# Performance work log

Measured on AMD Instinct MI355X. Metric: run time of the kernel, lower is better.

Reference implementation:

```python
import jax, jax.numpy as jnp
import numpy as np


def setup_inputs() -> dict:
    key = jax.random.key(0)
    k1, k2, k3, k4 = jax.random.split(key, 4)
    bs, h, qlen, slen, dk = 2, 16, 1024, 1024, 64
    q = jax.random.normal(k1, (bs, h, qlen, dk), dtype=jnp.float32)
    k = jax.random.normal(k2, (bs, h, dk, slen), dtype=jnp.float32)
    v = jax.random.normal(k3, (bs, h, slen, dk), dtype=jnp.float32)
    prev = jax.random.normal(k4, (bs, h, qlen, slen), dtype=jnp.float32)
    # scale param = head_dim ** -0.5 (lsa=False -> fixed, not trained)
    scale = jnp.asarray(dk ** (-0.5), dtype=jnp.float32)
    return {"q": q, "k": k, "v": v, "prev": prev, "scale": scale}


def reference(q, k, v, prev, scale):
    # attn_scores = (q @ k) * scale + prev   [bs, h, q_len, seq_len]
    attn_scores = jnp.einsum("bhqd,bhds->bhqs", q, k) * scale + prev
    # no attn_mask / key_padding_mask; dropout p=0.0 -> identity
    attn_weights = jax.nn.softmax(attn_scores, axis=-1)
    # output = attn_weights @ v   [bs, h, q_len, d_v]
    output = jnp.einsum("bhqs,bhsd->bhqd", attn_weights, v)
    # res_attention=True -> also return scores
    return output, attn_weights, attn_scores
```

## Files before the change

### kernel.cpp

```cpp
#include <hip/hip_runtime.h>
#include <hip/hip_bf16.h>

#define BH 32
#define L  1024
#define D  64
#define QT 16

typedef __bf16 bf16x8 __attribute__((ext_vector_type(8)));
typedef float  f32x4  __attribute__((ext_vector_type(4)));

__global__ __launch_bounds__(256) void prep_kernel(
    const float* __restrict__ q, const float* __restrict__ k,
    const float* __restrict__ v,
    __bf16* __restrict__ qb, __bf16* __restrict__ ktb, __bf16* __restrict__ vtb)
{
  __shared__ __align__(16) __bf16 T[128 * 66];
  const int tid = threadIdx.x;
  const int b = blockIdx.x;

  if (b < 1024) {
    const size_t g = (size_t)b * 256 + tid;
    const float4* qin = (const float4*)q;
    float4 f0 = qin[g * 2];
    float4 f1 = qin[g * 2 + 1];
    union { bf16x8 v8; uint4 u4; } o;
    o.v8[0] = (__bf16)f0.x; o.v8[1] = (__bf16)f0.y;
    o.v8[2] = (__bf16)f0.z; o.v8[3] = (__bf16)f0.w;
    o.v8[4] = (__bf16)f1.x; o.v8[5] = (__bf16)f1.y;
    o.v8[6] = (__bf16)f1.z; o.v8[7] = (__bf16)f1.w;
    *(uint4*)(qb + g * 8) = o.u4;
  } else if (b < 1280) {
    const int bb = b - 1024;
    const int bh = bb >> 3, chunk = bb & 7;
    const int s0 = chunk << 7;
    const float* kin = k + (size_t)bh * D * L;
    #pragma unroll
    for (int i = 0; i < 32; ++i) {
      const int e = i * 256 + tid;
      const int d = e >> 7, s = e & 127;
      T[s * 66 + d] = (__bf16)kin[(size_t)d * L + s0 + s];
    }
    __syncthreads();
    unsigned int* outw = (unsigned int*)ktb;
    const size_t obase = ((size_t)bh * L * D + (size_t)s0 * D) >> 1;
    #pragma unroll
    for (int i = 0; i < 16; ++i) {
      const int e = i * 256 + tid;
      const int s = e >> 5, dp = e & 31;
      outw[obase + e] = *(const unsigned int*)&T[s * 66 + dp * 2];
    }
  } else {
    const int bb = b - 1280;
    const int bh = bb >> 3, chunk = bb & 7;
    const int s0 = chunk << 7;
    const float* vin = v + (size_t)bh * L * D + (size_t)s0 * D;
    #pragma unroll
    for (int i = 0; i < 32; ++i) {
      const int e = i * 256 + tid;
      const int s = e >> 6, d = e & 63;
      T[d * 130 + s] = (__bf16)vin[e];
    }
    __syncthreads();
    unsigned int* outw = (unsigned int*)vtb;
    #pragma unroll
    for (int i = 0; i < 16; ++i) {
      const int e = i * 256 + tid;
      const int d = e >> 6, sp = e & 63;
      outw[(size_t)bh * (L * D / 2) + (size_t)d * (L / 2) + (s0 >> 1) + sp] =
          *(const unsigned int*)&T[d * 130 + sp * 2];
    }
  }
}

__global__ __launch_bounds__(256, 4) void attn_kernel(
    const __bf16* __restrict__ qb, const __bf16* __restrict__ ktb,
    const __bf16* __restrict__ vtb,
    const float* __restrict__ prev, const float* __restrict__ scale_p,
    float* __restrict__ out_o, float* __restrict__ out_w,
    float* __restrict__ out_s)
{
  __shared__ __align__(16) char smem[4 * 16 * 280 * 2];
  __shared__ float red_m[4][16];
  __shared__ float red_s[4][16];
  __bf16* w_stage = (__bf16*)smem;
  float*  o_red   = (float*)smem;

  const int tid  = threadIdx.x;
  const int wv   = tid >> 6;
  const int lane = tid & 63;
  const int quad = lane >> 4;
  const int l16  = lane & 15;
  const int bh   = blockIdx.x >> 6;
  const int qt   = blockIdx.x & 63;
  const float scale = scale_p[0];

  const __bf16* qtile = qb + ((size_t)bh * L + qt * QT) * D;
  const bf16x8 a0 = *(const bf16x8*)(qtile + l16 * D + quad * 8);
  const bf16x8 a1 = *(const bf16x8*)(qtile + l16 * D + 32 + quad * 8);

  const __bf16* kt_bh = ktb + (size_t)bh * L * D;
  const size_t row_base = (size_t)bh * L * L + (size_t)(qt * QT) * L;
  const int nbase = wv << 8;

  f32x4 p[16];
  const float* prow = prev + row_base + (size_t)(quad * 4) * L + nbase + l16;
  #pragma unroll
  for (int nt = 0; nt < 16; ++nt) {
    #pragma unroll
    for (int j = 0; j < 4; ++j)
      p[nt][j] = __builtin_nontemporal_load(prow + (size_t)j * L + nt * 16);
  }
  __builtin_amdgcn_sched_barrier(0);

  #pragma unroll
  for (int nt = 0; nt < 16; ++nt) {
    const int n0 = nbase + nt * 16;
    const __bf16* krow = kt_bh + (size_t)(n0 + l16) * D + quad * 8;
    const bf16x8 b0 = *(const bf16x8*)(krow);
    const bf16x8 b1 = *(const bf16x8*)(krow + 32);
    f32x4 c = {0.f, 0.f, 0.f, 0.f};
    c = __builtin_amdgcn_mfma_f32_16x16x32_bf16(a0, b0, c, 0, 0, 0);
    c = __builtin_amdgcn_mfma_f32_16x16x32_bf16(a1, b1, c, 0, 0, 0);
    #pragma unroll
    for (int j = 0; j < 4; ++j) {
      const size_t off = row_base + (size_t)(quad * 4 + j) * L + (n0 + l16);
      const float sc = c[j] * scale + p[nt][j];
      __builtin_nontemporal_store(sc, &out_s[off]);
      p[nt][j] = sc;
    }
  }

  float rm[4];
  #pragma unroll
  for (int j = 0; j < 4; ++j) {
    float m = p[0][j];
    #pragma unroll
    for (int nt = 1; nt < 16; ++nt) m = fmaxf(m, p[nt][j]);
    rm[j] = m;
  }
  #pragma unroll
  for (int sh = 1; sh < 16; sh <<= 1) {
    #pragma unroll
    for (int j = 0; j < 4; ++j) rm[j] = fmaxf(rm[j], __shfl_xor(rm[j], sh, 64));
  }
  if (l16 == 0) {
    #pragma unroll
    for (int j = 0; j < 4; ++j) red_m[wv][quad * 4 + j] = rm[j];
  }
  __syncthreads();
  #pragma unroll
  for (int j = 0; j < 4; ++j) {
    const int qr = quad * 4 + j;
    rm[j] = fmaxf(fmaxf(red_m[0][qr], red_m[1][qr]),
                  fmaxf(red_m[2][qr], red_m[3][qr]));
  }

  float rs[4] = {0.f, 0.f, 0.f, 0.f};
  #pragma unroll
  for (int nt = 0; nt < 16; ++nt) {
    #pragma unroll
    for (int j = 0; j < 4; ++j) {
      const float e = __expf(p[nt][j] - rm[j]);
      p[nt][j] = e;
      rs[j] += e;
    }
  }
  #pragma unroll
  for (int sh = 1; sh < 16; sh <<= 1) {
    #pragma unroll
    for (int j = 0; j < 4; ++j) rs[j] += __shfl_xor(rs[j], sh, 64);
  }
  if (l16 == 0) {
    #pragma unroll
    for (int j = 0; j < 4; ++j) red_s[wv][quad * 4 + j] = rs[j];
  }
  __syncthreads();
  #pragma unroll
  for (int j = 0; j < 4; ++j) {
    const int qr = quad * 4 + j;
    rs[j] = 1.0f / (red_s[0][qr] + red_s[1][qr] + red_s[2][qr] + red_s[3][qr]);
  }

  __bf16* wl = w_stage + wv * (16 * 280);
  #pragma unroll
  for (int nt = 0; nt < 16; ++nt) {
    #pragma unroll
    for (int j = 0; j < 4; ++j) {
      const int qr = quad * 4 + j;
      const float wt = p[nt][j] * rs[j];
      const size_t off = row_base + (size_t)qr * L + (nbase + nt * 16 + l16);
      __builtin_nontemporal_store(wt, &out_w[off]);
      wl[qr * 280 + nt * 16 + l16] = (__bf16)wt;
    }
  }

  const __bf16* vt_bh = vtb + (size_t)bh * D * L;
  f32x4 o[4];
  #pragma unroll
  for (int nt = 0; nt < 4; ++nt) o[nt] = (f32x4){0.f, 0.f, 0.f, 0.f};
  #pragma unroll
  for (int ks = 0; ks < 8; ++ks) {
    const bf16x8 aw = *(const bf16x8*)(wl + l16 * 280 + ks * 32 + quad * 8);
    #pragma unroll
    for (int nt = 0; nt < 4; ++nt) {
      const __bf16* vrow =
          vt_bh + (size_t)(nt * 16 + l16) * L + (nbase + ks * 32 + quad * 8);
      const bf16x8 bv = *(const bf16x8*)vrow;
      o[nt] = __builtin_amdgcn_mfma_f32_16x16x32_bf16(aw, bv, o[nt], 0, 0, 0);
    }
  }

  __syncthreads();
  #pragma unroll
  for (int nt = 0; nt < 4; ++nt) {
    #pragma unroll
    for (int j = 0; j < 4; ++j)
      o_red[wv * 1024 + (quad * 4 + j) * 64 + nt * 16 + l16] = o[nt][j];
  }
  __syncthreads();
  const size_t obase = (size_t)bh * L * D + (size_t)(qt * QT) * D;
  #pragma unroll
  for (int i = 0; i < 4; ++i) {
    const int idx = i * 256 + tid;
    const float sum =
        o_red[idx] + o_red[1024 + idx] + o_red[2048 + idx] + o_red[3072 + idx];
    out_o[obase + idx] = sum;
  }
}

extern "C" void kernel_launch(void* const* d_in, const int* in_sizes, int n_in,
                              void* d_out, int out_size, void* d_ws,
                              size_t ws_size, hipStream_t stream)
{
  const float* q     = (const float*)d_in[0];
  const float* k     = (const float*)d_in[1];
  const float* v     = (const float*)d_in[2];
  const float* prev  = (const float*)d_in[3];
  const float* scale = (const float*)d_in[4];

  float* out_o = (float*)d_out;
  float* out_w = out_o + (size_t)BH * L * D;
  float* out_s = out_w + (size_t)BH * L * L;

  __bf16* qb  = (__bf16*)d_ws;
  __bf16* ktb = qb + (size_t)BH * L * D;
  __bf16* vtb = ktb + (size_t)BH * L * D;

  prep_kernel<<<1536, 256, 0, stream>>>(q, k, v, qb, ktb, vtb);
  attn_kernel<<<2048, 256, 0, stream>>>(qb, ktb, vtb, prev, scale,
                                        out_o, out_w, out_s);
}
```

Measured before the change: 452.1 us.

## Swap MFMA operands for row-major vector I/O, fuse Q conversion, swizzle blocks

The QK^T MFMA operands are swapped so each lane holds four consecutive columns of one query row. This lets prev loads and score/weight stores use 16-byte vector accesses, and the row reductions simplify to two cross-quad shuffles. Q is now converted to bf16 inside the attention kernel, which removes that part of the prep kernel and its workspace round trip. The block index is swizzled and the LDS row pitch changes, which alters cache locality and bank-conflict patterns.

```diff
diff --git a/kernel.cpp b/kernel.cpp
--- a/kernel.cpp
+++ b/kernel.cpp
@@ -5,33 +5,22 @@
 #define L  1024
 #define D  64
 #define QT 16
+#define WROW 264
 
 typedef __bf16 bf16x8 __attribute__((ext_vector_type(8)));
+typedef __bf16 bf16x4 __attribute__((ext_vector_type(4)));
 typedef float  f32x4  __attribute__((ext_vector_type(4)));
 
 __global__ __launch_bounds__(256) void prep_kernel(
-    const float* __restrict__ q, const float* __restrict__ k,
-    const float* __restrict__ v,
-    __bf16* __restrict__ qb, __bf16* __restrict__ ktb, __bf16* __restrict__ vtb)
+    const float* __restrict__ k, const float* __restrict__ v,
+    __bf16* __restrict__ ktb, __bf16* __restrict__ vtb)
 {
   __shared__ __align__(16) __bf16 T[128 * 66];
   const int tid = threadIdx.x;
   const int b = blockIdx.x;
 
-  if (b < 1024) {
-    const size_t g = (size_t)b * 256 + tid;
-    const float4* qin = (const float4*)q;
-    float4 f0 = qin[g * 2];
-    float4 f1 = qin[g * 2 + 1];
-    union { bf16x8 v8; uint4 u4; } o;
-    o.v8[0] = (__bf16)f0.x; o.v8[1] = (__bf16)f0.y;
-    o.v8[2] = (__bf16)f0.z; o.v8[3] = (__bf16)f0.w;
-    o.v8[4] = (__bf16)f1.x; o.v8[5] = (__bf16)f1.y;
-    o.v8[6] = (__bf16)f1.z; o.v8[7] = (__bf16)f1.w;
-    *(uint4*)(qb + g * 8) = o.u4;
-  } else if (b < 1280) {
-    const int bb = b - 1024;
-    const int bh = bb >> 3, chunk = bb & 7;
+  if (b < 256) {
+    const int bh = b >> 3, chunk = b & 7;
     const int s0 = chunk << 7;
     const float* kin = k + (size_t)bh * D * L;
     #pragma unroll
@@ -50,7 +39,7 @@
       outw[obase + e] = *(const unsigned int*)&T[s * 66 + dp * 2];
     }
   } else {
-    const int bb = b - 1280;
+    const int bb = b - 256;
     const int bh = bb >> 3, chunk = bb & 7;
     const int s0 = chunk << 7;
     const float* vin = v + (size_t)bh * L * D + (size_t)s0 * D;
@@ -73,13 +62,13 @@
 }
 
 __global__ __launch_bounds__(256, 4) void attn_kernel(
-    const __bf16* __restrict__ qb, const __bf16* __restrict__ ktb,
+    const float* __restrict__ q, const __bf16* __restrict__ ktb,
     const __bf16* __restrict__ vtb,
     const float* __restrict__ prev, const float* __restrict__ scale_p,
     float* __restrict__ out_o, float* __restrict__ out_w,
     float* __restrict__ out_s)
 {
-  __shared__ __align__(16) char smem[4 * 16 * 280 * 2];
+  __shared__ __align__(16) char smem[4 * 16 * WROW * 2];
   __shared__ float red_m[4][16];
   __shared__ float red_s[4][16];
   __bf16* w_stage = (__bf16*)smem;
@@ -90,26 +79,32 @@
   const int lane = tid & 63;
   const int quad = lane >> 4;
   const int l16  = lane & 15;
-  const int bh   = blockIdx.x >> 6;
-  const int qt   = blockIdx.x & 63;
+
+  const int swz = (blockIdx.x & 7) * 256 + (blockIdx.x >> 3);
+  const int bh  = swz >> 6;
+  const int qt  = swz & 63;
   const float scale = scale_p[0];
 
-  const __bf16* qtile = qb + ((size_t)bh * L + qt * QT) * D;
-  const bf16x8 a0 = *(const bf16x8*)(qtile + l16 * D + quad * 8);
-  const bf16x8 a1 = *(const bf16x8*)(qtile + l16 * D + 32 + quad * 8);
+  const float* qr0 = q + ((size_t)bh * L + qt * QT + l16) * D + quad * 8;
+  const float4 f0 = *(const float4*)(qr0);
+  const float4 f1 = *(const float4*)(qr0 + 4);
+  const float4 f2 = *(const float4*)(qr0 + 32);
+  const float4 f3 = *(const float4*)(qr0 + 36);
+  bf16x8 a0, a1;
+  a0[0] = (__bf16)f0.x; a0[1] = (__bf16)f0.y; a0[2] = (__bf16)f0.z; a0[3] = (__bf16)f0.w;
+  a0[4] = (__bf16)f1.x; a0[5] = (__bf16)f1.y; a0[6] = (__bf16)f1.z; a0[7] = (__bf16)f1.w;
+  a1[0] = (__bf16)f2.x; a1[1] = (__bf16)f2.y; a1[2] = (__bf16)f2.z; a1[3] = (__bf16)f2.w;
+  a1[4] = (__bf16)f3.x; a1[5] = (__bf16)f3.y; a1[6] = (__bf16)f3.z; a1[7] = (__bf16)f3.w;
 
   const __bf16* kt_bh = ktb + (size_t)bh * L * D;
   const size_t row_base = (size_t)bh * L * L + (size_t)(qt * QT) * L;
   const int nbase = wv << 8;
 
   f32x4 p[16];
-  const float* prow = prev + row_base + (size_t)(quad * 4) * L + nbase + l16;
-  #pragma unroll
-  for (int nt = 0; nt < 16; ++nt) {
-    #pragma unroll
-    for (int j = 0; j < 4; ++j)
-      p[nt][j] = __builtin_nontemporal_load(prow + (size_t)j * L + nt * 16);
-  }
+  const float* prow = prev + row_base + (size_t)l16 * L + nbase + quad * 4;
+  #pragma unroll
+  for (int nt = 0; nt < 16; ++nt)
+    p[nt] = __builtin_nontemporal_load((const f32x4*)(prow + nt * 16));
   __builtin_amdgcn_sched_barrier(0);
 
   #pragma unroll
@@ -119,79 +114,63 @@
     const bf16x8 b0 = *(const bf16x8*)(krow);
     const bf16x8 b1 = *(const bf16x8*)(krow + 32);
     f32x4 c = {0.f, 0.f, 0.f, 0.f};
-    c = __builtin_amdgcn_mfma_f32_16x16x32_bf16(a0, b0, c, 0, 0, 0);
-    c = __builtin_amdgcn_mfma_f32_16x16x32_bf16(a1, b1, c, 0, 0, 0);
-    #pragma unroll
-    for (int j = 0; j < 4; ++j) {
-      const size_t off = row_base + (size_t)(quad * 4 + j) * L + (n0 + l16);
-      const float sc = c[j] * scale + p[nt][j];
-      __builtin_nontemporal_store(sc, &out_s[off]);
-      p[nt][j] = sc;
-    }
-  }
-
-  float rm[4];
+    c = __builtin_amdgcn_mfma_f32_16x16x32_bf16(b0, a0, c, 0, 0, 0);
+    c = __builtin_amdgcn_mfma_f32_16x16x32_bf16(b1, a1, c, 0, 0, 0);
+    f32x4 sc;
+    #pragma unroll
+    for (int j = 0; j < 4; ++j) sc[j] = c[j] * scale + p[nt][j];
+    __builtin_nontemporal_store(
+        sc, (f32x4*)(out_s + row_base + (size_t)l16 * L + n0 + quad * 4));
+    p[nt] = sc;
+  }
+
+  float mj[4];
   #pragma unroll
   for (int j = 0; j < 4; ++j) {
     float m = p[0][j];
     #pragma unroll
     for (int nt = 1; nt < 16; ++nt) m = fmaxf(m, p[nt][j]);
-    rm[j] = m;
-  }
-  #pragma unroll
-  for (int sh = 1; sh < 16; sh <<= 1) {
-    #pragma unroll
-    for (int j = 0; j < 4; ++j) rm[j] = fmaxf(rm[j], __shfl_xor(rm[j], sh, 64));
-  }
-  if (l16 == 0) {
-    #pragma unroll
-    for (int j = 0; j < 4; ++j) red_m[wv][quad * 4 + j] = rm[j];
-  }
-  __syncthreads();
-  #pragma unroll
-  for (int j = 0; j < 4; ++j) {
-    const int qr = quad * 4 + j;
-    rm[j] = fmaxf(fmaxf(red_m[0][qr], red_m[1][qr]),
-                  fmaxf(red_m[2][qr], red_m[3][qr]));
-  }
-
-  float rs[4] = {0.f, 0.f, 0.f, 0.f};
+    mj[j] = m;
+  }
+  float m = fmaxf(fmaxf(mj[0], mj[1]), fmaxf(mj[2], mj[3]));
+  m = fmaxf(m, __shfl_xor(m, 16, 64));
+  m = fmaxf(m, __shfl_xor(m, 32, 64));
+  if (lane < 16) red_m[wv][l16] = m;
+  __syncthreads();
+  m = fmaxf(fmaxf(red_m[0][l16], red_m[1][l16]),
+            fmaxf(red_m[2][l16], red_m[3][l16]));
+
+  float sj[4] = {0.f, 0.f, 0.f, 0.f};
   #pragma unroll
   for (int nt = 0; nt < 16; ++nt) {
     #pragma unroll
     for (int j = 0; j < 4; ++j) {
-      const float e = __expf(p[nt][j] - rm[j]);
+      const float e = __expf(p[nt][j] - m);
       p[nt][j] = e;
-      rs[j] += e;
-    }
-  }
-  #pragma unroll
-  for (int sh = 1; sh < 16; sh <<= 1) {
-    #pragma unroll
-    for (int j = 0; j < 4; ++j) rs[j] += __shfl_xor(rs[j], sh, 64);
-  }
-  if (l16 == 0) {
-    #pragma unroll
-    for (int j = 0; j < 4; ++j) red_s[wv][quad * 4 + j] = rs[j];
-  }
-  __syncthreads();
-  #pragma unroll
-  for (int j = 0; j < 4; ++j) {
-    const int qr = quad * 4 + j;
-    rs[j] = 1.0f / (red_s[0][qr] + red_s[1][qr] + red_s[2][qr] + red_s[3][qr]);
-  }
-
-  __bf16* wl = w_stage + wv * (16 * 280);
+      sj[j] += e;
+    }
+  }
+  float s = (sj[0] + sj[1]) + (sj[2] + sj[3]);
+  s += __shfl_xor(s, 16, 64);
+  s += __shfl_xor(s, 32, 64);
+  if (lane < 16) red_s[wv][l16] = s;
+  __syncthreads();
+  const float inv =
+      1.0f / (red_s[0][l16] + red_s[1][l16] + red_s[2][l16] + red_s[3][l16]);
+
+  __bf16* wl = w_stage + wv * (16 * WROW);
   #pragma unroll
   for (int nt = 0; nt < 16; ++nt) {
+    f32x4 wt;
+    bf16x4 wb;
     #pragma unroll
     for (int j = 0; j < 4; ++j) {
-      const int qr = quad * 4 + j;
-      const float wt = p[nt][j] * rs[j];
-      const size_t off = row_base + (size_t)qr * L + (nbase + nt * 16 + l16);
-      __builtin_nontemporal_store(wt, &out_w[off]);
-      wl[qr * 280 + nt * 16 + l16] = (__bf16)wt;
-    }
+      wt[j] = p[nt][j] * inv;
+      wb[j] = (__bf16)wt[j];
+    }
+    __builtin_nontemporal_store(
+        wt, (f32x4*)(out_w + row_base + (size_t)l16 * L + nbase + nt * 16 + quad * 4));
+    *(bf16x4*)(wl + l16 * WROW + nt * 16 + quad * 4) = wb;
   }
 
   const __bf16* vt_bh = vtb + (size_t)bh * D * L;
@@ -200,7 +179,7 @@
   for (int nt = 0; nt < 4; ++nt) o[nt] = (f32x4){0.f, 0.f, 0.f, 0.f};
   #pragma unroll
   for (int ks = 0; ks < 8; ++ks) {
-    const bf16x8 aw = *(const bf16x8*)(wl + l16 * 280 + ks * 32 + quad * 8);
+    const bf16x8 aw = *(const bf16x8*)(wl + l16 * WROW + ks * 32 + quad * 8);
     #pragma unroll
     for (int nt = 0; nt < 4; ++nt) {
       const __bf16* vrow =
@@ -242,11 +221,10 @@
   float* out_w = out_o + (size_t)BH * L * D;
   float* out_s = out_w + (size_t)BH * L * L;
 
-  __bf16* qb  = (__bf16*)d_ws;
-  __bf16* ktb = qb + (size_t)BH * L * D;
+  __bf16* ktb = (__bf16*)d_ws;
   __bf16* vtb = ktb + (size_t)BH * L * D;
 
-  prep_kernel<<<1536, 256, 0, stream>>>(q, k, v, qb, ktb, vtb);
-  attn_kernel<<<2048, 256, 0, stream>>>(qb, ktb, vtb, prev, scale,
+  prep_kernel<<<512, 256, 0, stream>>>(k, v, ktb, vtb);
+  attn_kernel<<<2048, 256, 0, stream>>>(q, ktb, vtb, prev, scale,
                                         out_o, out_w, out_s);
 }
```

Result: no change. 453.5 us (+0.3%).
